# Kernel tuning notes

Measured on AMD Instinct MI355X. Metric: run time of the kernel, lower is better.

Reference implementation:

```python
import jax, jax.numpy as jnp
import numpy as np

H, HKV, D = 8, 1, 256  # query heads, kv heads, head_dim (Gemma-2B-like)


def apply_rope(x, sin, cos):
    # x: [B, h, D, S]; sin/cos: [B, 1, D//2, S]
    x1, x2 = jnp.split(x, 2, axis=-2)
    return jnp.concatenate((x1 * cos - x2 * sin, x2 * cos + x1 * sin), axis=-2)


def setup_inputs() -> dict:
    key = jax.random.key(0)
    ks = jax.random.split(key, 12)
    B, hidden, S = 2, 2048, 2048
    half = D // 2
    Xq = jax.random.normal(ks[0], (B, hidden, S), jnp.float32)
    Xkv = jax.random.normal(ks[1], (B, hidden, S), jnp.float32)
    sin_q = jax.random.uniform(ks[2], (B, 1, half, S), jnp.float32, -1.0, 1.0)
    cos_q = jax.random.uniform(ks[3], (B, 1, half, S), jnp.float32, -1.0, 1.0)
    sin_k = jax.random.uniform(ks[4], (B, 1, half, S), jnp.float32, -1.0, 1.0)
    cos_k = jax.random.uniform(ks[5], (B, 1, half, S), jnp.float32, -1.0, 1.0)
    attn_mask = jnp.zeros((B, 1, S, S), jnp.float32)
    scale = 0.02
    Wq = jax.random.normal(ks[6], (H * D, hidden), jnp.float32) * scale
    Wk = jax.random.normal(ks[7], (HKV * D, hidden), jnp.float32) * scale
    Wv = jax.random.normal(ks[8], (HKV * D, hidden), jnp.float32) * scale
    Wo = jax.random.normal(ks[9], (hidden, H * D), jnp.float32) * scale
    return {"Xq": Xq, "Xkv": Xkv, "sin_q": sin_q, "cos_q": cos_q,
            "sin_k": sin_k, "cos_k": cos_k, "attn_mask": attn_mask,
            "Wq": Wq, "Wk": Wk, "Wv": Wv, "Wo": Wo}


def reference(Xq, Xkv, sin_q, cos_q, sin_k, cos_k, attn_mask, Wq, Wk, Wv, Wo):
    B, hidden, Sq = Xq.shape
    Sk = Xkv.shape[-1]
    # ANEDenseGeneral = 1x1 conv over channels-first layout
    q = jnp.einsum('oc,bcs->bos', Wq, Xq).reshape(B, H, D, Sq)
    q = apply_rope(q, sin_q, cos_q)
    k = jnp.einsum('oc,bcs->bos', Wk, Xkv).reshape(B, HKV, D, Sk)
    k = apply_rope(k, sin_k, cos_k)
    v = jnp.einsum('oc,bcs->bos', Wv, Xkv).reshape(B, HKV, D, Sk)
    # GQA: broadcast kv heads to query heads
    rep = H // HKV
    k = jnp.repeat(k, rep, axis=1)
    v = jnp.repeat(v, rep, axis=1)
    scale = 1.0 / jnp.sqrt(jnp.asarray(D, Xq.dtype))
    scores = jnp.einsum('bhdq,bhdk->bhqk', q, k) * scale + attn_mask
    probs = jax.nn.softmax(scores, axis=-1)
    out = jnp.einsum('bhqk,bhdk->bhdq', probs, v).reshape(B, H * D, Sq)
    return jnp.einsum('oc,bcs->bos', Wo, out).astype(Xq.dtype)
```

## Files before the change

### kernel.cpp

```cpp
#include <hip/hip_runtime.h>

typedef __bf16 bf16;
typedef __bf16 bf16x8 __attribute__((ext_vector_type(8)));
typedef __bf16 bf16x4 __attribute__((ext_vector_type(4)));
typedef float f32x4 __attribute__((ext_vector_type(4)));

static constexpr int Hh = 8;
static constexpr int Dd = 256;
static constexpr int Ss = 2048;
static constexpr int Cc = 2048;

typedef const __attribute__((address_space(1))) unsigned int as1_u32;
typedef __attribute__((address_space(3))) unsigned int as3_u32;

__device__ __forceinline__ void gl_lds16(const void* g, void* l) {
  __builtin_amdgcn_global_load_lds((as1_u32*)(unsigned long long)g,
                                   (as3_u32*)(unsigned int)(unsigned long long)l,
                                   16, 0, 0);
}

__device__ __forceinline__ f32x4 mfma16(bf16x8 a, bf16x8 b, f32x4 c) {
  return __builtin_amdgcn_mfma_f32_16x16x32_bf16(a, b, c, 0, 0, 0);
}

__global__ __launch_bounds__(256) void cvt_w(const float* __restrict__ in,
                                             bf16* __restrict__ out, int n) {
  int i = (blockIdx.x * 256 + threadIdx.x) * 4;
  if (i >= n) return;
  const float4 v = *(const float4*)(in + i);
  bf16x4 o;
  o[0] = (bf16)v.x; o[1] = (bf16)v.y; o[2] = (bf16)v.z; o[3] = (bf16)v.w;
  *(bf16x4*)(out + i) = o;
}

__global__ __launch_bounds__(256) void transpose_cvt(const float* __restrict__ in,
                                                     bf16* __restrict__ out,
                                                     int R, int S) {
  __shared__ float t[32][33];
  const int b = blockIdx.z;
  const long base = (long)b * R * S;
  const int s0 = blockIdx.x * 32, r0 = blockIdx.y * 32;
  const int tx = threadIdx.x, ty = threadIdx.y;
#pragma unroll
  for (int i = 0; i < 32; i += 8)
    t[ty + i][tx] = in[base + (long)(r0 + ty + i) * S + s0 + tx];
  __syncthreads();
#pragma unroll
  for (int i = 0; i < 32; i += 8)
    out[base + (long)(s0 + ty + i) * R + r0 + tx] = (bf16)t[tx][ty + i];
}

__global__ __launch_bounds__(256) void rope_transpose(
    const bf16* __restrict__ xin, const bf16* __restrict__ sint,
    const bf16* __restrict__ cost, bf16* __restrict__ xout, int nH,
    long bStr) {
  __shared__ __align__(16) bf16 ti[32][264];
  const int b = blockIdx.z, h = blockIdx.y, s0 = blockIdx.x * 32;
  const int tx = threadIdx.x, ty = threadIdx.y;
  const bf16* src = xin + (long)b * bStr + (long)h * Dd * Ss + s0;
#pragma unroll
  for (int i = 0; i < 32; ++i) {
    int d = ty + i * 8;
    ti[tx][d] = src[(long)d * Ss + tx];
  }
  __syncthreads();
  const int t = ty * 32 + tx;
  const int s = t >> 3;
  const int dpart = t & 7;
  const bf16* sp = sint + ((long)b * Ss + s0 + s) * 128;
  const bf16* cp = cost + ((long)b * Ss + s0 + s) * 128;
  bf16* dst = xout + (((long)(b * nH + h)) * Ss + s0 + s) * Dd;
#pragma unroll
  for (int i = 0; i < 4; ++i) {
    int d0 = dpart * 8 + i * 64;
    int dh = d0 & 127;
    bf16x8 a = *(const bf16x8*)&ti[s][d0];
    bf16x8 p = *(const bf16x8*)&ti[s][(d0 < 128) ? d0 + 128 : d0 - 128];
    bf16x8 sn = *(const bf16x8*)&sp[dh];
    bf16x8 cs = *(const bf16x8*)&cp[dh];
    bf16x8 o;
#pragma unroll
    for (int j = 0; j < 8; ++j) {
      float av = (float)a[j], pv = (float)p[j];
      float c = (float)cs[j], sv = (float)sn[j];
      float val = (d0 < 128) ? (av * c - pv * sv) : (av * c + pv * sv);
      o[j] = (bf16)val;
    }
    *(bf16x8*)&dst[d0] = o;
  }
}

__global__ __launch_bounds__(256, 2) void gemm_bt(
    const bf16* __restrict__ A, const bf16* __restrict__ Bt,
    bf16* __restrict__ Cb, float* __restrict__ Cf, int M, int N, int K,
    long sBt, long sC) {
  __shared__ __align__(16) bf16 lA[2][128 * 64];
  __shared__ __align__(16) bf16 lB[2][128 * 64];
  const int tid = threadIdx.x;
  const int wid = tid >> 6, lane = tid & 63;
  const int g = lane >> 4, r = lane & 15;
  const int wr = wid >> 1, wc = wid & 1;
  const int mt = blockIdx.y * 128, nt = blockIdx.x * 128;
  const int z = blockIdx.z;
  const bf16* Bz = Bt + (long)z * sBt;

  auto stage = [&](int buf, int kt) {
#pragma unroll
    for (int it = 0; it < 4; ++it) {
      int off = it * 4096 + tid * 16;
      int row = off >> 7;
      int c = (off >> 4) & 7;
      int csw = c ^ (row & 7);
      gl_lds16((const char*)(A + (long)(mt + row) * K + kt) + csw * 16,
               (char*)lA[buf] + it * 4096 + wid * 1024);
      gl_lds16((const char*)(Bz + (long)(nt + row) * K + kt) + csw * 16,
               (char*)lB[buf] + it * 4096 + wid * 1024);
    }
  };

  const f32x4 zf = {0.f, 0.f, 0.f, 0.f};
  f32x4 acc[4][4];
#pragma unroll
  for (int m = 0; m < 4; ++m)
#pragma unroll
    for (int n = 0; n < 4; ++n) acc[m][n] = zf;

  stage(0, 0);
  __syncthreads();
  int cur = 0;
  for (int kt = 0; kt < K; kt += 64) {
    if (kt + 64 < K) stage(cur ^ 1, kt + 64);
#pragma unroll
    for (int kk = 0; kk < 2; ++kk) {
      bf16x8 af[4], bfv[4];
#pragma unroll
      for (int m = 0; m < 4; ++m) {
        int row = wr * 64 + m * 16 + r;
        int csw = (kk * 4 + g) ^ (row & 7);
        af[m] = *(const bf16x8*)((const char*)lA[cur] + row * 128 + csw * 16);
      }
#pragma unroll
      for (int n = 0; n < 4; ++n) {
        int row = wc * 64 + n * 16 + r;
        int csw = (kk * 4 + g) ^ (row & 7);
        bfv[n] = *(const bf16x8*)((const char*)lB[cur] + row * 128 + csw * 16);
      }
#pragma unroll
      for (int m = 0; m < 4; ++m)
#pragma unroll
        for (int n = 0; n < 4; ++n)
          acc[m][n] = mfma16(af[m], bfv[n], acc[m][n]);
    }
    __syncthreads();
    cur ^= 1;
  }

#pragma unroll
  for (int m = 0; m < 4; ++m)
#pragma unroll
    for (int n = 0; n < 4; ++n)
#pragma unroll
      for (int e = 0; e < 4; ++e) {
        int orow = mt + wr * 64 + m * 16 + g * 4 + e;
        int col = nt + wc * 64 + n * 16 + r;
        long idx = (long)z * sC + (long)orow * N + col;
        if (Cf) Cf[idx] = acc[m][n][e];
        else Cb[idx] = (bf16)acc[m][n][e];
      }
}

__global__ __launch_bounds__(256, 2) void attn_kernel(
    const bf16* __restrict__ qr, const bf16* __restrict__ kr,
    const bf16* __restrict__ kv, const float* __restrict__ mask,
    bf16* __restrict__ aout) {
  __shared__ __align__(16) bf16 lK[2][32 * 256];
  __shared__ __align__(16) bf16 lV[2][256 * 32];
  __shared__ __align__(16) bf16 lP[4][16 * 40];
  const int b = blockIdx.z, hg = blockIdx.y;
  const int q0 = blockIdx.x * 16;
  const int tid = threadIdx.x;
  const int wid = tid >> 6, lane = tid & 63;
  const int g = lane >> 4, q = lane & 15;
  const int h = hg * 4 + wid;

  bf16x8 qf[8];
  const bf16* qp = qr + (((long)(b * Hh + h)) * Ss + q0 + q) * Dd;
#pragma unroll
  for (int kk = 0; kk < 8; ++kk) qf[kk] = *(const bf16x8*)&qp[kk * 32 + g * 8];

  const f32x4 zf = {0.f, 0.f, 0.f, 0.f};
  f32x4 oacc[16];
#pragma unroll
  for (int i = 0; i < 16; ++i) oacc[i] = zf;
  float mrun = -3e38f, lrun = 0.f;

  const char* kb = (const char*)(kr + (long)b * Ss * Dd);
  const char* vb = (const char*)(kv + ((long)b * 2 * Dd + Dd) * Ss);
  const float* mb = mask + (long)b * Ss * Ss;

  auto stage = [&](int buf, int kt) {
    const char* gK = kb + (long)kt * 512;
#pragma unroll
    for (int it = 0; it < 4; ++it) {
      int off = it * 4096 + tid * 16;
      int row = off >> 9;
      int c = (off >> 4) & 31;
      int csw = c ^ (row & 7);
      gl_lds16(gK + row * 512 + csw * 16,
               (char*)lK[buf] + it * 4096 + wid * 1024);
    }
#pragma unroll
    for (int it = 0; it < 4; ++it) {
      int off = it * 4096 + tid * 16;
      int row = off >> 6;
      int c = (off >> 4) & 3;
      int csw = c ^ ((row >> 1) & 3);
      gl_lds16(vb + (long)row * (Ss * 2) + (long)kt * 2 + csw * 16,
               (char*)lV[buf] + it * 4096 + wid * 1024);
    }
  };

  stage(0, 0);
  __syncthreads();
  int cur = 0;

  for (int kt = 0; kt < Ss; kt += 32) {
    if (kt + 32 < Ss) stage(cur ^ 1, kt + 32);

    const float* mrow = mb + (long)(q0 + q) * Ss + kt;
    const float4 mv0 = *(const float4*)(mrow + 4 * g);
    const float4 mv1 = *(const float4*)(mrow + 16 + 4 * g);

    f32x4 sacc[2] = {zf, zf};
    __builtin_amdgcn_s_setprio(1);
#pragma unroll
    for (int kk = 0; kk < 8; ++kk) {
#pragma unroll
      for (int n = 0; n < 2; ++n) {
        int row = n * 16 + q;
        int csw = (kk * 4 + g) ^ (row & 7);
        bf16x8 kf = *(const bf16x8*)((const char*)lK[cur] + row * 512 + csw * 16);
        sacc[n] = mfma16(kf, qf[kk], sacc[n]);
      }
    }
    __builtin_amdgcn_s_setprio(0);

    float x[8];
    x[0] = sacc[0][0] * 0.0625f + mv0.x;
    x[1] = sacc[0][1] * 0.0625f + mv0.y;
    x[2] = sacc[0][2] * 0.0625f + mv0.z;
    x[3] = sacc[0][3] * 0.0625f + mv0.w;
    x[4] = sacc[1][0] * 0.0625f + mv1.x;
    x[5] = sacc[1][1] * 0.0625f + mv1.y;
    x[6] = sacc[1][2] * 0.0625f + mv1.z;
    x[7] = sacc[1][3] * 0.0625f + mv1.w;
    float mx = fmaxf(fmaxf(fmaxf(x[0], x[1]), fmaxf(x[2], x[3])),
                     fmaxf(fmaxf(x[4], x[5]), fmaxf(x[6], x[7])));
    mx = fmaxf(mx, __shfl_xor(mx, 16, 64));
    mx = fmaxf(mx, __shfl_xor(mx, 32, 64));
    if (mx > mrun + 8.0f) {
      float al = __expf(mrun - mx);
      lrun *= al;
#pragma unroll
      for (int nf = 0; nf < 16; ++nf) oacc[nf] *= al;
      mrun = mx;
    }
    float p[8];
    float rs = 0.f;
#pragma unroll
    for (int i = 0; i < 8; ++i) {
      p[i] = __expf(x[i] - mrun);
      rs += p[i];
    }
    rs += __shfl_xor(rs, 16, 64);
    rs += __shfl_xor(rs, 32, 64);
    lrun += rs;

    bf16x4 w0, w1;
#pragma unroll
    for (int e = 0; e < 4; ++e) { w0[e] = (bf16)p[e]; w1[e] = (bf16)p[4 + e]; }
    *(bf16x4*)&lP[wid][q * 40 + 4 * g] = w0;
    *(bf16x4*)&lP[wid][q * 40 + 16 + 4 * g] = w1;

    bf16x8 pf = *(const bf16x8*)&lP[wid][q * 40 + g * 8];
    __builtin_amdgcn_s_setprio(1);
#pragma unroll
    for (int nf = 0; nf < 16; ++nf) {
      int row = nf * 16 + q;
      int csw = g ^ ((row >> 1) & 3);
      bf16x8 vf = *(const bf16x8*)((const char*)lV[cur] + row * 64 + csw * 16);
      oacc[nf] = mfma16(vf, pf, oacc[nf]);
    }
    __builtin_amdgcn_s_setprio(0);

    __syncthreads();
    cur ^= 1;
  }

  const float inv = 1.f / lrun;
  bf16* op = aout + ((long)(b * Ss + q0 + q)) * (Hh * Dd) + h * Dd + g * 4;
#pragma unroll
  for (int nf = 0; nf < 16; ++nf) {
    bf16x4 o4;
#pragma unroll
    for (int e = 0; e < 4; ++e) o4[e] = (bf16)(oacc[nf][e] * inv);
    *(bf16x4*)&op[nf * 16] = o4;
  }
}

extern "C" void kernel_launch(void* const* d_in, const int* in_sizes, int n_in,
                              void* d_out, int out_size, void* d_ws,
                              size_t ws_size, hipStream_t stream) {
  const float* Xq = (const float*)d_in[0];
  const float* Xkv = (const float*)d_in[1];
  const float* sin_q = (const float*)d_in[2];
  const float* cos_q = (const float*)d_in[3];
  const float* sin_k = (const float*)d_in[4];
  const float* cos_k = (const float*)d_in[5];
  const float* mask = (const float*)d_in[6];
  const float* Wq = (const float*)d_in[7];
  const float* Wk = (const float*)d_in[8];
  const float* Wv = (const float*)d_in[9];
  const float* Wo = (const float*)d_in[10];
  float* out = (float*)d_out;

  char* ws = (char*)d_ws;
  const size_t MB = 1u << 20;
  bf16* Wq_bf = (bf16*)(ws + 0 * MB);
  bf16* Wo_bf = (bf16*)(ws + 8 * MB);
  bf16* Wkv_bf = (bf16*)(ws + 16 * MB);
  bf16* Wv_bf = (bf16*)(ws + 17 * MB);
  bf16* sin_qt = (bf16*)(ws + 18 * MB);
  bf16* cos_qt = (bf16*)(ws + 19 * MB);
  bf16* sin_kt = (bf16*)(ws + 20 * MB);
  bf16* cos_kt = (bf16*)(ws + 21 * MB);
  bf16* Xtq = (bf16*)(ws + 22 * MB);
  bf16* Xtkv = (bf16*)(ws + 38 * MB);
  bf16* q_tmp = (bf16*)(ws + 54 * MB);
  bf16* kv_tmp = (bf16*)(ws + 70 * MB);
  bf16* qr = (bf16*)(ws + 22 * MB);
  bf16* kr = (bf16*)(ws + 38 * MB);
  bf16* attnb = (bf16*)(ws + 54 * MB);

  dim3 b256(256), b32x8(32, 8);

  cvt_w<<<4096, b256, 0, stream>>>(Wq, Wq_bf, Cc * Cc);
  cvt_w<<<4096, b256, 0, stream>>>(Wo, Wo_bf, Cc * Cc);
  cvt_w<<<512, b256, 0, stream>>>(Wk, (bf16*)Wkv_bf, Dd * Cc);
  cvt_w<<<512, b256, 0, stream>>>(Wv, Wv_bf, Dd * Cc);

  transpose_cvt<<<dim3(64, 64, 2), b32x8, 0, stream>>>(Xq, Xtq, Cc, Ss);
  transpose_cvt<<<dim3(64, 64, 2), b32x8, 0, stream>>>(Xkv, Xtkv, Cc, Ss);
  transpose_cvt<<<dim3(64, 4, 2), b32x8, 0, stream>>>(sin_q, sin_qt, 128, Ss);
  transpose_cvt<<<dim3(64, 4, 2), b32x8, 0, stream>>>(cos_q, cos_qt, 128, Ss);
  transpose_cvt<<<dim3(64, 4, 2), b32x8, 0, stream>>>(sin_k, sin_kt, 128, Ss);
  transpose_cvt<<<dim3(64, 4, 2), b32x8, 0, stream>>>(cos_k, cos_kt, 128, Ss);

  gemm_bt<<<dim3(16, 16, 2), b256, 0, stream>>>(
      Wq_bf, Xtq, q_tmp, nullptr, Cc, Ss, Cc, (long)Ss * Cc, (long)Cc * Ss);
  gemm_bt<<<dim3(16, 4, 2), b256, 0, stream>>>(
      Wkv_bf, Xtkv, kv_tmp, nullptr, 2 * Dd, Ss, Cc, (long)Ss * Cc,
      (long)2 * Dd * Ss);

  rope_transpose<<<dim3(64, 8, 2), b32x8, 0, stream>>>(
      q_tmp, sin_qt, cos_qt, qr, Hh, (long)Hh * Dd * Ss);
  rope_transpose<<<dim3(64, 1, 2), b32x8, 0, stream>>>(
      kv_tmp, sin_kt, cos_kt, kr, 1, (long)2 * Dd * Ss);

  attn_kernel<<<dim3(128, 2, 2), b256, 0, stream>>>(qr, kr, kv_tmp, mask,
                                                    attnb);

  gemm_bt<<<dim3(16, 16, 2), b256, 0, stream>>>(
      Wo_bf, attnb, nullptr, out, Cc, Ss, Cc, (long)Ss * Cc, (long)Cc * Ss);
}
```

Measured before the change: 283.6 us.

## Merge batch into GEMM N dimension with XCD-aware tile remap; drop setprio

The projection GEMMs now treat both batches as one wider N dimension (4096 columns), so the intermediate q/kv layouts become [rows, B*S] and rope/attention indexing is adjusted to the new row stride. Block IDs are remapped so consecutive tiles land on the same XCD, improving L2 reuse of the shared weight tiles, and the output GEMM scatters columns back to per-batch layout. The s_setprio hints around the MFMA loops in attention are also removed. The flat grid and remap assume the grid size is a multiple of 8.

```diff
diff --git a/kernel.cpp b/kernel.cpp
--- a/kernel.cpp
+++ b/kernel.cpp
@@ -9,6 +9,7 @@
 static constexpr int Dd = 256;
 static constexpr int Ss = 2048;
 static constexpr int Cc = 2048;
+static constexpr int NS = 4096;
 
 typedef const __attribute__((address_space(1))) unsigned int as1_u32;
 typedef __attribute__((address_space(3))) unsigned int as3_u32;
@@ -53,15 +54,15 @@
 __global__ __launch_bounds__(256) void rope_transpose(
     const bf16* __restrict__ xin, const bf16* __restrict__ sint,
     const bf16* __restrict__ cost, bf16* __restrict__ xout, int nH,
-    long bStr) {
+    long bOff, long rowStr) {
   __shared__ __align__(16) bf16 ti[32][264];
   const int b = blockIdx.z, h = blockIdx.y, s0 = blockIdx.x * 32;
   const int tx = threadIdx.x, ty = threadIdx.y;
-  const bf16* src = xin + (long)b * bStr + (long)h * Dd * Ss + s0;
+  const bf16* src = xin + b * bOff + (long)h * Dd * rowStr + s0;
 #pragma unroll
   for (int i = 0; i < 32; ++i) {
     int d = ty + i * 8;
-    ti[tx][d] = src[(long)d * Ss + tx];
+    ti[tx][d] = src[(long)d * rowStr + tx];
   }
   __syncthreads();
   const int t = ty * 32 + tx;
@@ -93,16 +94,17 @@
 __global__ __launch_bounds__(256, 2) void gemm_bt(
     const bf16* __restrict__ A, const bf16* __restrict__ Bt,
     bf16* __restrict__ Cb, float* __restrict__ Cf, int M, int N, int K,
-    long sBt, long sC) {
+    int ntiles) {
   __shared__ __align__(16) bf16 lA[2][128 * 64];
   __shared__ __align__(16) bf16 lB[2][128 * 64];
+  const int nwg = gridDim.x;
+  const int cpx = nwg >> 3;
+  const int bid2 = (blockIdx.x & 7) * cpx + (blockIdx.x >> 3);
+  const int mt = (bid2 / ntiles) * 128, nt = (bid2 % ntiles) * 128;
   const int tid = threadIdx.x;
   const int wid = tid >> 6, lane = tid & 63;
   const int g = lane >> 4, r = lane & 15;
   const int wr = wid >> 1, wc = wid & 1;
-  const int mt = blockIdx.y * 128, nt = blockIdx.x * 128;
-  const int z = blockIdx.z;
-  const bf16* Bz = Bt + (long)z * sBt;
 
   auto stage = [&](int buf, int kt) {
 #pragma unroll
@@ -113,7 +115,7 @@
       int csw = c ^ (row & 7);
       gl_lds16((const char*)(A + (long)(mt + row) * K + kt) + csw * 16,
                (char*)lA[buf] + it * 4096 + wid * 1024);
-      gl_lds16((const char*)(Bz + (long)(nt + row) * K + kt) + csw * 16,
+      gl_lds16((const char*)(Bt + (long)(nt + row) * K + kt) + csw * 16,
                (char*)lB[buf] + it * 4096 + wid * 1024);
     }
   };
@@ -163,9 +165,13 @@
       for (int e = 0; e < 4; ++e) {
         int orow = mt + wr * 64 + m * 16 + g * 4 + e;
         int col = nt + wc * 64 + n * 16 + r;
-        long idx = (long)z * sC + (long)orow * N + col;
-        if (Cf) Cf[idx] = acc[m][n][e];
-        else Cb[idx] = (bf16)acc[m][n][e];
+        if (Cf) {
+          long idx = (long)(col >> 11) * ((long)Cc * Ss) + (long)orow * Ss +
+                     (col & 2047);
+          Cf[idx] = acc[m][n][e];
+        } else {
+          Cb[(long)orow * N + col] = (bf16)acc[m][n][e];
+        }
       }
 }
 
@@ -195,7 +201,7 @@
   float mrun = -3e38f, lrun = 0.f;
 
   const char* kb = (const char*)(kr + (long)b * Ss * Dd);
-  const char* vb = (const char*)(kv + ((long)b * 2 * Dd + Dd) * Ss);
+  const char* vb = (const char*)(kv + (long)256 * NS + (long)b * Ss);
   const float* mb = mask + (long)b * Ss * Ss;
 
   auto stage = [&](int buf, int kt) {
@@ -215,7 +221,7 @@
       int row = off >> 6;
       int c = (off >> 4) & 3;
       int csw = c ^ ((row >> 1) & 3);
-      gl_lds16(vb + (long)row * (Ss * 2) + (long)kt * 2 + csw * 16,
+      gl_lds16(vb + (long)row * (NS * 2) + (long)kt * 2 + csw * 16,
                (char*)lV[buf] + it * 4096 + wid * 1024);
     }
   };
@@ -232,7 +238,6 @@
     const float4 mv1 = *(const float4*)(mrow + 16 + 4 * g);
 
     f32x4 sacc[2] = {zf, zf};
-    __builtin_amdgcn_s_setprio(1);
 #pragma unroll
     for (int kk = 0; kk < 8; ++kk) {
 #pragma unroll
@@ -243,7 +248,6 @@
         sacc[n] = mfma16(kf, qf[kk], sacc[n]);
       }
     }
-    __builtin_amdgcn_s_setprio(0);
 
     float x[8];
     x[0] = sacc[0][0] * 0.0625f + mv0.x;
@@ -283,7 +287,6 @@
     *(bf16x4*)&lP[wid][q * 40 + 16 + 4 * g] = w1;
 
     bf16x8 pf = *(const bf16x8*)&lP[wid][q * 40 + g * 8];
-    __builtin_amdgcn_s_setprio(1);
 #pragma unroll
     for (int nf = 0; nf < 16; ++nf) {
       int row = nf * 16 + q;
@@ -291,7 +294,6 @@
       bf16x8 vf = *(const bf16x8*)((const char*)lV[cur] + row * 64 + csw * 16);
       oacc[nf] = mfma16(vf, pf, oacc[nf]);
     }
-    __builtin_amdgcn_s_setprio(0);
 
     __syncthreads();
     cur ^= 1;
@@ -356,20 +358,19 @@
   transpose_cvt<<<dim3(64, 4, 2), b32x8, 0, stream>>>(sin_k, sin_kt, 128, Ss);
   transpose_cvt<<<dim3(64, 4, 2), b32x8, 0, stream>>>(cos_k, cos_kt, 128, Ss);
 
-  gemm_bt<<<dim3(16, 16, 2), b256, 0, stream>>>(
-      Wq_bf, Xtq, q_tmp, nullptr, Cc, Ss, Cc, (long)Ss * Cc, (long)Cc * Ss);
-  gemm_bt<<<dim3(16, 4, 2), b256, 0, stream>>>(
-      Wkv_bf, Xtkv, kv_tmp, nullptr, 2 * Dd, Ss, Cc, (long)Ss * Cc,
-      (long)2 * Dd * Ss);
+  gemm_bt<<<dim3(512), b256, 0, stream>>>(Wq_bf, Xtq, q_tmp, nullptr,
+                                          Cc, NS, Cc, NS / 128);
+  gemm_bt<<<dim3(128), b256, 0, stream>>>(Wkv_bf, Xtkv, kv_tmp, nullptr,
+                                          2 * Dd, NS, Cc, NS / 128);
 
   rope_transpose<<<dim3(64, 8, 2), b32x8, 0, stream>>>(
-      q_tmp, sin_qt, cos_qt, qr, Hh, (long)Hh * Dd * Ss);
+      q_tmp, sin_qt, cos_qt, qr, Hh, (long)Ss, (long)NS);
   rope_transpose<<<dim3(64, 1, 2), b32x8, 0, stream>>>(
-      kv_tmp, sin_kt, cos_kt, kr, 1, (long)2 * Dd * Ss);
+      kv_tmp, sin_kt, cos_kt, kr, 1, (long)Ss, (long)NS);
 
   attn_kernel<<<dim3(128, 2, 2), b256, 0, stream>>>(qr, kr, kv_tmp, mask,
                                                     attnb);
 
-  gemm_bt<<<dim3(16, 16, 2), b256, 0, stream>>>(
-      Wo_bf, attnb, nullptr, out, Cc, Ss, Cc, (long)Ss * Cc, (long)Cc * Ss);
-}
+  gemm_bt<<<dim3(512), b256, 0, stream>>>(Wo_bf, attnb, nullptr, out,
+                                          Cc, NS, Cc, NS / 128);
+}
```

After: 292.1 us. +3.0%, slower.
